# Kernel optimization log

Hardware: AMD Instinct MI355X
Metric: run time of the kernel (lower is better)

Reference implementation:

```python
import jax, jax.numpy as jnp
import numpy as np
import math

N_HEAD = 16  # from init_kwargs

def setup_inputs() -> dict:
    key = jax.random.key(0)
    ks = jax.random.split(key, 11)
    B, T, D = 2, 2048, 1024
    s = 0.02
    return {
        "q": jax.random.normal(ks[0], (B, T, D), jnp.float32),
        "k": jax.random.normal(ks[1], (B, T, D), jnp.float32),
        "v": jax.random.normal(ks[2], (B, T, D), jnp.float32),
        "Wq": jax.random.normal(ks[3], (D, D), jnp.float32) * s,
        "bq": jax.random.normal(ks[4], (D,), jnp.float32) * s,
        "Wk": jax.random.normal(ks[5], (D, D), jnp.float32) * s,
        "bk": jax.random.normal(ks[6], (D,), jnp.float32) * s,
        "Wv": jax.random.normal(ks[7], (D, D), jnp.float32) * s,
        "bv": jax.random.normal(ks[8], (D,), jnp.float32) * s,
        "Wc": jax.random.normal(ks[9], (D, D), jnp.float32) * s,
        "bc": jax.random.normal(ks[10], (D,), jnp.float32) * s,
    }

def reference(q, k, v, Wq, bq, Wk, bk, Wv, bv, Wc, bc):
    B, T, D = q.shape
    H = N_HEAD
    nd = D // H

    def proj(x, W, b):
        # torch Linear: x @ W.T + b; then split heads -> [b, h, t, nd]
        y = x @ W.T + b
        return y.reshape(B, T, H, nd).transpose(0, 2, 1, 3)

    qh = proj(q, Wq, bq)
    kh = proj(k, Wk, bk)
    vh = proj(v, Wv, bv)

    # scores: [b, h, t_q, t_k]
    z = jnp.einsum('bhqd,bhkd->bhqk', qh, kh) / math.sqrt(nd)
    mask = jnp.tril(jnp.ones((T, T), dtype=bool))  # causal
    z = jnp.where(mask, z, -jnp.inf)
    # NOTE: original uses nn.Softmax(dim=-2) -> softmax over the QUERY axis
    attn = jax.nn.softmax(z, axis=-2)
    out = jnp.einsum('bhqk,bhkd->bhqd', attn, vh)  # [b, h, t, nd]
    out = out.transpose(0, 2, 1, 3).reshape(B, T, D)
    return out @ Wc.T + bc
```

## Files before the change

### kernel.cpp

```cpp
#include <hip/hip_runtime.h>


#define Dd 1024
#define Tt 2048
#define Bb 2
#define Hh 16
#define NDh 64
#define Mm (Bb * Tt)

using u16 = unsigned short;
using u32 = unsigned int;
typedef __attribute__((ext_vector_type(8))) short bf16x8;
typedef __attribute__((ext_vector_type(4))) float f32x4;

__device__ __forceinline__ u16 f2bf(float f) {
  return (u16)((__float_as_uint(f) + 0x8000u) >> 16);
}
__device__ __forceinline__ u32 pk2(float a, float b) {
  u32 ua = __float_as_uint(a) + 0x8000u;
  u32 ub = __float_as_uint(b) + 0x8000u;
  return __builtin_amdgcn_perm(ub, ua, 0x07060302u);
}
__device__ __forceinline__ void ldsdma16(const u16* g, u16* l) {
  __builtin_amdgcn_global_load_lds(
      (const __attribute__((address_space(1))) u32*)g,
      (__attribute__((address_space(3))) u32*)l, 16, 0, 0);
}
#define MFMA(a, b, c) __builtin_amdgcn_mfma_f32_16x16x32_bf16((a), (b), (c), 0, 0, 0)
__device__ __forceinline__ bf16x8 ldfrag(const u16* lds, int row, int kgrp) {
  return *(const bf16x8*)(lds + row * 64 + (((kgrp) ^ (row & 7)) * 8));
}

__global__ __launch_bounds__(256) void cvt_w(
    const float* __restrict__ w0, const float* __restrict__ w1,
    const float* __restrict__ w2, const float* __restrict__ w3,
    u16* __restrict__ dst, float* __restrict__ outz, float* __restrict__ lsumz)
{
  const int vid = blockIdx.x * 256 + threadIdx.x;
  const int seg = vid >> 18;
  const int off = (vid & 0x3FFFF) * 4;
  const float* s = seg == 0 ? w0 : seg == 1 ? w1 : seg == 2 ? w2 : w3;
  float4 f = *(const float4*)(s + off);
  ushort4 o;
  o.x = f2bf(f.x); o.y = f2bf(f.y); o.z = f2bf(f.z); o.w = f2bf(f.w);
  *(ushort4*)(dst + (size_t)seg * Dd * Dd + off) = o;
  *(float4*)(outz + (size_t)vid * 4) = make_float4(0.f, 0.f, 0.f, 0.f);
  if (vid < Bb * Hh * Tt / 4)
    *(float4*)(lsumz + (size_t)vid * 4) = make_float4(0.f, 0.f, 0.f, 0.f);
}

template <bool XF32>
__device__ __forceinline__ void gemm_body(
    const void* Xv, const u16* __restrict__ WB, const float* __restrict__ bias,
    void* Yv, float oscale, int omode, int kc, int knum, u16* As, u16* Bs)
{
  const int t = threadIdx.x, lane = t & 63, w = t >> 6;
  const int col = lane & 15, quad = lane >> 4;
  const int m0 = blockIdx.x * 64, n0 = blockIdx.y * 128;
  const int wm = (w >> 1) * 32, wn = (w & 1) * 64;
  const int drr = lane >> 3, dsw = ((lane & 7) ^ drr) * 8;
  const int ar = t >> 2, ag = (t & 3) * 2;
  const int kbeg = (Dd / knum) * kc, kend = kbeg + Dd / knum;

  f32x4 acc[2][4] = {};
  float4 xf[4];
  const float* X32 = (const float*)Xv;
  if constexpr (XF32) {
#pragma unroll
    for (int j = 0; j < 4; j++)
      xf[j] = ((const float4*)(X32 + (size_t)(m0 + ar) * Dd + kbeg + ag * 8))[j];
  }

  for (int k0 = kbeg; k0 < kend; k0 += 64) {
    __syncthreads();
#pragma unroll
    for (int i = 0; i < 4; i++) {
      const int rr = w * 32 + i * 8;
      ldsdma16(WB + (size_t)(n0 + rr + drr) * Dd + k0 + dsw, Bs + rr * 64);
    }
    if constexpr (XF32) {
      u32 pk[8];
#pragma unroll
      for (int j = 0; j < 4; j++) {
        pk[2 * j]     = pk2(xf[j].x, xf[j].y);
        pk[2 * j + 1] = pk2(xf[j].z, xf[j].w);
      }
      u16* dst = As + ar * 64;
      *(uint4*)(dst + ((ag ^ (ar & 7)) * 8))       = make_uint4(pk[0], pk[1], pk[2], pk[3]);
      *(uint4*)(dst + (((ag + 1) ^ (ar & 7)) * 8)) = make_uint4(pk[4], pk[5], pk[6], pk[7]);
      if (k0 + 64 < kend) {
#pragma unroll
        for (int j = 0; j < 4; j++)
          xf[j] = ((const float4*)(X32 + (size_t)(m0 + ar) * Dd + k0 + 64 + ag * 8))[j];
      }
    } else {
      const u16* X = (const u16*)Xv;
#pragma unroll
      for (int i = 0; i < 2; i++) {
        const int rr = w * 16 + i * 8;
        ldsdma16(X + (size_t)(m0 + rr + drr) * Dd + k0 + dsw, As + rr * 64);
      }
    }
    __syncthreads();
#pragma unroll
    for (int s = 0; s < 2; s++) {
      bf16x8 a[2], b[4];
#pragma unroll
      for (int i = 0; i < 2; i++)
        a[i] = ldfrag(As, wm + i * 16 + col, s * 4 + quad);
#pragma unroll
      for (int j = 0; j < 4; j++)
        b[j] = ldfrag(Bs, wn + j * 16 + col, s * 4 + quad);
#pragma unroll
      for (int i = 0; i < 2; i++)
#pragma unroll
        for (int j = 0; j < 4; j++)
          acc[i][j] = MFMA(a[i], b[j], acc[i][j]);
    }
  }

#pragma unroll
  for (int jt = 0; jt < 4; jt++) {
    const int n = n0 + wn + jt * 16 + col;
    const float bn = (omode == 2 && kc != 0) ? 0.f : bias[n];
    if (omode == 1) {
#pragma unroll
      for (int i = 0; i < 2; i++) {
        const int mg = m0 + wm + i * 16 + quad * 4;
        const int bb = mg >> 11, tl = mg & 2047;
        ushort4 o;
        o.x = f2bf(acc[i][jt][0] + bn);
        o.y = f2bf(acc[i][jt][1] + bn);
        o.z = f2bf(acc[i][jt][2] + bn);
        o.w = f2bf(acc[i][jt][3] + bn);
        *(ushort4*)((u16*)Yv + (size_t)bb * Dd * Tt + (size_t)n * Tt + tl) = o;
      }
    } else if (omode == 0) {
      u16* Y = (u16*)Yv;
#pragma unroll
      for (int i = 0; i < 2; i++)
#pragma unroll
        for (int r = 0; r < 4; r++) {
          const int m = m0 + wm + i * 16 + quad * 4 + r;
          Y[(size_t)m * Dd + n] = f2bf((acc[i][jt][r] + bn) * oscale);
        }
    } else {
      float* Y = (float*)Yv;
#pragma unroll
      for (int i = 0; i < 2; i++)
#pragma unroll
        for (int r = 0; r < 4; r++) {
          const int m = m0 + wm + i * 16 + quad * 4 + r;
          atomicAdd(&Y[(size_t)m * Dd + n], acc[i][jt][r] + bn);
        }
    }
  }
}

__global__ __launch_bounds__(256) void proj_qkv(
    const float* __restrict__ q, const float* __restrict__ k,
    const float* __restrict__ v, const u16* __restrict__ Wb,
    const float* __restrict__ bq, const float* __restrict__ bk,
    const float* __restrict__ bv,
    u16* __restrict__ Qp, u16* __restrict__ Kp, u16* __restrict__ VtG)
{
  __shared__ u16 As[64 * 64];
  __shared__ u16 Bs[128 * 64];
  const int z = blockIdx.z;
  const float* X = z == 0 ? q : z == 1 ? k : v;
  const u16* W = Wb + (size_t)z * Dd * Dd;
  const float* bias = z == 0 ? bq : z == 1 ? bk : bv;
  void* Y = z == 0 ? (void*)Qp : z == 1 ? (void*)Kp : (void*)VtG;
  gemm_body<true>(X, W, bias, Y, z == 0 ? 0.125f : 1.0f, z == 2 ? 1 : 0, 0, 1, As, Bs);
}

__global__ __launch_bounds__(256) void gemm_final(
    const u16* __restrict__ Ctx, const u16* __restrict__ Wcb,
    const float* __restrict__ bc, float* __restrict__ out)
{
  __shared__ u16 As[64 * 64];
  __shared__ u16 Bs[128 * 64];
  gemm_body<false>(Ctx, Wcb, bc, out, 1.0f, 2, blockIdx.z, 2, As, Bs);
}

__global__ __launch_bounds__(256) void attn_stats(
    const u16* __restrict__ Qp, const u16* __restrict__ Kp,
    float* __restrict__ lsum)
{
  __shared__ u16 Ks[128 * 64];
  __shared__ u16 Qs[64 * 64];
  const int t = threadIdx.x, lane = t & 63, w = t >> 6;
  const int col = lane & 15, quad = lane >> 4;
  const int bh = blockIdx.x, b = bh >> 4, h = bh & 15;
  const int j = blockIdx.y, tk0 = j * 128, c = blockIdx.z;
  const u16* Kbase = Kp + (size_t)b * Tt * Dd + h * NDh;
  const u16* Qbase = Qp + (size_t)b * Tt * Dd + h * NDh;
  const int drr = lane >> 3, dsw = ((lane & 7) ^ drr) * 8;

#pragma unroll
  for (int i = 0; i < 4; i++) {
    const int rr = w * 32 + i * 8;
    ldsdma16(Kbase + (size_t)(tk0 + rr + drr) * Dd + dsw, Ks + rr * 64);
  }
  __syncthreads();
  bf16x8 ka[2][2];
#pragma unroll
  for (int s2 = 0; s2 < 2; s2++) {
    const int row = w * 32 + s2 * 16 + col;
    ka[s2][0] = ldfrag(Ks, row, quad);
    ka[s2][1] = ldfrag(Ks, row, 4 + quad);
  }

  float l[2][4] = {};

  for (int d = 2 * j + c, i0 = 0; d < Tt / 64; d += 4, i0++) {
    const bool masked = (c < 2) && (i0 == 0);
    const int tq0 = d * 64;
    __syncthreads();
#pragma unroll
    for (int i = 0; i < 2; i++) {
      const int rr = w * 16 + i * 8;
      ldsdma16(Qbase + (size_t)(tq0 + rr + drr) * Dd + dsw, Qs + rr * 64);
    }
    __syncthreads();
#pragma unroll
    for (int jt = 0; jt < 4; jt++) {
      bf16x8 qb0 = ldfrag(Qs, jt * 16 + col, quad);
      bf16x8 qb1 = ldfrag(Qs, jt * 16 + col, 4 + quad);
      const int tq = tq0 + jt * 16 + col;
#pragma unroll
      for (int s2 = 0; s2 < 2; s2++) {
        f32x4 z = {};
        z = MFMA(ka[s2][0], qb0, z);
        z = MFMA(ka[s2][1], qb1, z);
#pragma unroll
        for (int r = 0; r < 4; r++) {
          float e = __expf(z[r]);
          if (masked) {
            const int tk = tk0 + w * 32 + s2 * 16 + quad * 4 + r;
            e = (tq >= tk) ? e : 0.f;
          }
          l[s2][r] += e;
        }
      }
    }
  }

#pragma unroll
  for (int s2 = 0; s2 < 2; s2++)
#pragma unroll
    for (int r = 0; r < 4; r++) {
      float s = l[s2][r];
#pragma unroll
      for (int m = 1; m < 16; m <<= 1) s += __shfl_xor(s, m);
      if (col == 0)
        atomicAdd(&lsum[(size_t)bh * Tt + tk0 + w * 32 + s2 * 16 + quad * 4 + r], s);
    }
}

__global__ __launch_bounds__(256) void attn_out(
    const u16* __restrict__ Qp, const u16* __restrict__ Kp,
    const u16* __restrict__ VtG, const float* __restrict__ lsum,
    u16* __restrict__ Ctx)
{
  __shared__ u16 QPs[64 * 64];
  __shared__ u16 Ks[64 * 64];
  __shared__ u16 Vts[64 * 64];
  __shared__ float srl[64];
  const int t = threadIdx.x, lane = t & 63, w = t >> 6;
  const int col = lane & 15, quad = lane >> 4;
  const int bh = blockIdx.x, b = bh >> 4, h = bh & 15;
  const int tq0 = (gridDim.y - 1 - blockIdx.y) * 64;
  const u16* Qbase = Qp + (size_t)b * Tt * Dd + h * NDh;
  const u16* Kbase = Kp + (size_t)b * Tt * Dd + h * NDh;
  const u16* Vbase = VtG + (size_t)b * Dd * Tt + (size_t)h * NDh * Tt;
  const int drr = lane >> 3, dsw = ((lane & 7) ^ drr) * 8;

#pragma unroll
  for (int i = 0; i < 2; i++) {
    const int rr = w * 16 + i * 8;
    ldsdma16(Qbase + (size_t)(tq0 + rr + drr) * Dd + dsw, QPs + rr * 64);
  }
  __syncthreads();
  bf16x8 qa[2];
  qa[0] = ldfrag(QPs, w * 16 + col, quad);
  qa[1] = ldfrag(QPs, w * 16 + col, 4 + quad);

  f32x4 o[4] = {};

  for (int tk0 = 0; tk0 <= tq0; tk0 += 64) {
    const bool masked = (tk0 == tq0);
    __syncthreads();
#pragma unroll
    for (int i = 0; i < 2; i++) {
      const int rr = w * 16 + i * 8;
      ldsdma16(Kbase + (size_t)(tk0 + rr + drr) * Dd + dsw, Ks + rr * 64);
      ldsdma16(Vbase + (size_t)(rr + drr) * Tt + tk0 + dsw, Vts + rr * 64);
    }
    if (t < 64) srl[t] = 1.0f / lsum[(size_t)bh * Tt + tk0 + t];
    __syncthreads();
#pragma unroll
    for (int jt = 0; jt < 4; jt++) {
      bf16x8 kb0 = ldfrag(Ks, jt * 16 + col, quad);
      bf16x8 kb1 = ldfrag(Ks, jt * 16 + col, 4 + quad);
      const int tkl = jt * 16 + col;
      const float rl = srl[tkl];
      f32x4 z = {};
      z = MFMA(qa[0], kb0, z);
      z = MFMA(qa[1], kb1, z);
#pragma unroll
      for (int r = 0; r < 4; r++) {
        const int row = w * 16 + quad * 4 + r;
        float p = __expf(z[r]) * rl;
        if (masked) p = (tkl <= row) ? p : 0.f;
        QPs[row * 64 + (((tkl >> 3) ^ (row & 7)) * 8) + (tkl & 7)] = f2bf(p);
      }
    }
    bf16x8 pa0 = ldfrag(QPs, w * 16 + col, quad);
    bf16x8 pa1 = ldfrag(QPs, w * 16 + col, 4 + quad);
#pragma unroll
    for (int dn = 0; dn < 4; dn++) {
      bf16x8 vb0 = ldfrag(Vts, dn * 16 + col, quad);
      bf16x8 vb1 = ldfrag(Vts, dn * 16 + col, 4 + quad);
      o[dn] = MFMA(pa0, vb0, o[dn]);
      o[dn] = MFMA(pa1, vb1, o[dn]);
    }
  }

#pragma unroll
  for (int dn = 0; dn < 4; dn++)
#pragma unroll
    for (int r = 0; r < 4; r++) {
      const int tq = tq0 + w * 16 + quad * 4 + r;
      Ctx[(size_t)(b * Tt + tq) * Dd + h * NDh + dn * 16 + col] = f2bf(o[dn][r]);
    }
}

extern "C" void kernel_launch(void* const* d_in, const int* in_sizes, int n_in,
                              void* d_out, int out_size, void* d_ws, size_t ws_size,
                              hipStream_t stream)
{
  const float* q  = (const float*)d_in[0];
  const float* k  = (const float*)d_in[1];
  const float* v  = (const float*)d_in[2];
  const float* Wq = (const float*)d_in[3];
  const float* bq = (const float*)d_in[4];
  const float* Wk = (const float*)d_in[5];
  const float* bk = (const float*)d_in[6];
  const float* Wv = (const float*)d_in[7];
  const float* bv = (const float*)d_in[8];
  const float* Wc = (const float*)d_in[9];
  const float* bc = (const float*)d_in[10];

  u16* Wb   = (u16*)d_ws;
  u16* Qp   = Wb + (size_t)4 * Dd * Dd;
  u16* Kp   = Qp + (size_t)Mm * Dd;
  u16* VtG  = Kp + (size_t)Mm * Dd;
  u16* Ctx  = VtG + (size_t)Mm * Dd;
  float* lsum = (float*)(Ctx + (size_t)Mm * Dd);

  cvt_w<<<4096, 256, 0, stream>>>(Wq, Wk, Wv, Wc, Wb, (float*)d_out, lsum);
  proj_qkv<<<dim3(Mm / 64, Dd / 128, 3), 256, 0, stream>>>(
      q, k, v, Wb, bq, bk, bv, Qp, Kp, VtG);
  attn_stats<<<dim3(Bb * Hh, Tt / 128, 4), 256, 0, stream>>>(Qp, Kp, lsum);
  attn_out<<<dim3(Bb * Hh, Tt / 64), 256, 0, stream>>>(Qp, Kp, VtG, lsum, Ctx);
  gemm_final<<<dim3(Mm / 64, Dd / 128, 2), 256, 0, stream>>>(
      Ctx, Wb + (size_t)3 * Dd * Dd, bc, (float*)d_out);
}
```

Measured before the change: 268.0 us.

## Pre-convert activations to bf16 and use 128x128 GEMM tiles with LDS DMA

Activation conversion from fp32 to bf16 for q/k/v moves into the weight-conversion kernel, so the projection GEMM can load both operands with global-to-LDS DMA instead of register-staged conversion. GEMM tiles for both projection and final GEMMs grow from 64x128 to 128x128, giving each wave a 64x64 sub-tile and more MFMA work per loaded byte. This costs an extra bf16 round trip of the activations through memory and more registers per thread, and it reuses workspace regions (Ctx holds converted v) which must not conflict in time. Grid sizes halve, which lowers the number of concurrent blocks.

```diff
diff --git a/kernel.cpp b/kernel.cpp
--- a/kernel.cpp
+++ b/kernel.cpp
@@ -16,11 +16,6 @@
 __device__ __forceinline__ u16 f2bf(float f) {
   return (u16)((__float_as_uint(f) + 0x8000u) >> 16);
 }
-__device__ __forceinline__ u32 pk2(float a, float b) {
-  u32 ua = __float_as_uint(a) + 0x8000u;
-  u32 ub = __float_as_uint(b) + 0x8000u;
-  return __builtin_amdgcn_perm(ub, ua, 0x07060302u);
-}
 __device__ __forceinline__ void ldsdma16(const u16* g, u16* l) {
   __builtin_amdgcn_global_load_lds(
       (const __attribute__((address_space(1))) u32*)g,
@@ -31,88 +26,72 @@
   return *(const bf16x8*)(lds + row * 64 + (((kgrp) ^ (row & 7)) * 8));
 }
 
-__global__ __launch_bounds__(256) void cvt_w(
+__global__ __launch_bounds__(256) void cvt_all(
     const float* __restrict__ w0, const float* __restrict__ w1,
     const float* __restrict__ w2, const float* __restrict__ w3,
-    u16* __restrict__ dst, float* __restrict__ outz, float* __restrict__ lsumz)
+    const float* __restrict__ xq, const float* __restrict__ xk,
+    const float* __restrict__ xv,
+    u16* __restrict__ Wb, u16* __restrict__ Qb, u16* __restrict__ Kb,
+    u16* __restrict__ Vb, float* __restrict__ outz, float* __restrict__ lsumz)
 {
   const int vid = blockIdx.x * 256 + threadIdx.x;
   const int seg = vid >> 18;
-  const int off = (vid & 0x3FFFF) * 4;
-  const float* s = seg == 0 ? w0 : seg == 1 ? w1 : seg == 2 ? w2 : w3;
+  const size_t off = (size_t)(vid & 0x3FFFF) * 4;
+  const float* s;
+  u16* d;
+  if (seg < 4) {
+    s = seg == 0 ? w0 : seg == 1 ? w1 : seg == 2 ? w2 : w3;
+    d = Wb + (size_t)seg * Dd * Dd;
+  } else {
+    const int xi = (seg - 4) >> 2;
+    const size_t xo = (size_t)((seg - 4) & 3) << 20;
+    s = (xi == 0 ? xq : xi == 1 ? xk : xv) + xo;
+    d = (xi == 0 ? Qb : xi == 1 ? Kb : Vb) + xo;
+  }
   float4 f = *(const float4*)(s + off);
   ushort4 o;
   o.x = f2bf(f.x); o.y = f2bf(f.y); o.z = f2bf(f.z); o.w = f2bf(f.w);
-  *(ushort4*)(dst + (size_t)seg * Dd * Dd + off) = o;
-  *(float4*)(outz + (size_t)vid * 4) = make_float4(0.f, 0.f, 0.f, 0.f);
+  *(ushort4*)(d + off) = o;
+  if (vid < Mm * Dd / 4)
+    *(float4*)(outz + (size_t)vid * 4) = make_float4(0.f, 0.f, 0.f, 0.f);
   if (vid < Bb * Hh * Tt / 4)
     *(float4*)(lsumz + (size_t)vid * 4) = make_float4(0.f, 0.f, 0.f, 0.f);
 }
 
-template <bool XF32>
 __device__ __forceinline__ void gemm_body(
-    const void* Xv, const u16* __restrict__ WB, const float* __restrict__ bias,
-    void* Yv, float oscale, int omode, int kc, int knum, u16* As, u16* Bs)
+    const u16* __restrict__ X, const u16* __restrict__ WB,
+    const float* __restrict__ bias, void* Yv, float oscale, int omode,
+    int kc, int knum, u16* As, u16* Bs)
 {
   const int t = threadIdx.x, lane = t & 63, w = t >> 6;
   const int col = lane & 15, quad = lane >> 4;
-  const int m0 = blockIdx.x * 64, n0 = blockIdx.y * 128;
-  const int wm = (w >> 1) * 32, wn = (w & 1) * 64;
+  const int m0 = blockIdx.x * 128, n0 = blockIdx.y * 128;
+  const int wm = (w >> 1) * 64, wn = (w & 1) * 64;
   const int drr = lane >> 3, dsw = ((lane & 7) ^ drr) * 8;
-  const int ar = t >> 2, ag = (t & 3) * 2;
   const int kbeg = (Dd / knum) * kc, kend = kbeg + Dd / knum;
 
-  f32x4 acc[2][4] = {};
-  float4 xf[4];
-  const float* X32 = (const float*)Xv;
-  if constexpr (XF32) {
-#pragma unroll
-    for (int j = 0; j < 4; j++)
-      xf[j] = ((const float4*)(X32 + (size_t)(m0 + ar) * Dd + kbeg + ag * 8))[j];
-  }
+  f32x4 acc[4][4] = {};
 
   for (int k0 = kbeg; k0 < kend; k0 += 64) {
     __syncthreads();
 #pragma unroll
     for (int i = 0; i < 4; i++) {
       const int rr = w * 32 + i * 8;
+      ldsdma16(X  + (size_t)(m0 + rr + drr) * Dd + k0 + dsw, As + rr * 64);
       ldsdma16(WB + (size_t)(n0 + rr + drr) * Dd + k0 + dsw, Bs + rr * 64);
     }
-    if constexpr (XF32) {
-      u32 pk[8];
-#pragma unroll
-      for (int j = 0; j < 4; j++) {
-        pk[2 * j]     = pk2(xf[j].x, xf[j].y);
-        pk[2 * j + 1] = pk2(xf[j].z, xf[j].w);
-      }
-      u16* dst = As + ar * 64;
-      *(uint4*)(dst + ((ag ^ (ar & 7)) * 8))       = make_uint4(pk[0], pk[1], pk[2], pk[3]);
-      *(uint4*)(dst + (((ag + 1) ^ (ar & 7)) * 8)) = make_uint4(pk[4], pk[5], pk[6], pk[7]);
-      if (k0 + 64 < kend) {
-#pragma unroll
-        for (int j = 0; j < 4; j++)
-          xf[j] = ((const float4*)(X32 + (size_t)(m0 + ar) * Dd + k0 + 64 + ag * 8))[j];
-      }
-    } else {
-      const u16* X = (const u16*)Xv;
-#pragma unroll
-      for (int i = 0; i < 2; i++) {
-        const int rr = w * 16 + i * 8;
-        ldsdma16(X + (size_t)(m0 + rr + drr) * Dd + k0 + dsw, As + rr * 64);
-      }
-    }
     __syncthreads();
 #pragma unroll
     for (int s = 0; s < 2; s++) {
-      bf16x8 a[2], b[4];
-#pragma unroll
-      for (int i = 0; i < 2; i++)
+      bf16x8 a[4], b[4];
+#pragma unroll
+      for (int i = 0; i < 4; i++)
         a[i] = ldfrag(As, wm + i * 16 + col, s * 4 + quad);
 #pragma unroll
       for (int j = 0; j < 4; j++)
         b[j] = ldfrag(Bs, wn + j * 16 + col, s * 4 + quad);
 #pragma unroll
-      for (int i = 0; i < 2; i++)
+      for (int i = 0; i < 4; i++)
 #pragma unroll
         for (int j = 0; j < 4; j++)
           acc[i][j] = MFMA(a[i], b[j], acc[i][j]);
@@ -125,7 +104,7 @@
     const float bn = (omode == 2 && kc != 0) ? 0.f : bias[n];
     if (omode == 1) {
 #pragma unroll
-      for (int i = 0; i < 2; i++) {
+      for (int i = 0; i < 4; i++) {
         const int mg = m0 + wm + i * 16 + quad * 4;
         const int bb = mg >> 11, tl = mg & 2047;
         ushort4 o;
@@ -138,7 +117,7 @@
     } else if (omode == 0) {
       u16* Y = (u16*)Yv;
 #pragma unroll
-      for (int i = 0; i < 2; i++)
+      for (int i = 0; i < 4; i++)
 #pragma unroll
         for (int r = 0; r < 4; r++) {
           const int m = m0 + wm + i * 16 + quad * 4 + r;
@@ -147,7 +126,7 @@
     } else {
       float* Y = (float*)Yv;
 #pragma unroll
-      for (int i = 0; i < 2; i++)
+      for (int i = 0; i < 4; i++)
 #pragma unroll
         for (int r = 0; r < 4; r++) {
           const int m = m0 + wm + i * 16 + quad * 4 + r;
@@ -158,29 +137,29 @@
 }
 
 __global__ __launch_bounds__(256) void proj_qkv(
-    const float* __restrict__ q, const float* __restrict__ k,
-    const float* __restrict__ v, const u16* __restrict__ Wb,
+    const u16* __restrict__ Qb, const u16* __restrict__ Kb,
+    const u16* __restrict__ Vb, const u16* __restrict__ Wb,
     const float* __restrict__ bq, const float* __restrict__ bk,
     const float* __restrict__ bv,
     u16* __restrict__ Qp, u16* __restrict__ Kp, u16* __restrict__ VtG)
 {
-  __shared__ u16 As[64 * 64];
+  __shared__ u16 As[128 * 64];
   __shared__ u16 Bs[128 * 64];
   const int z = blockIdx.z;
-  const float* X = z == 0 ? q : z == 1 ? k : v;
+  const u16* X = z == 0 ? Qb : z == 1 ? Kb : Vb;
   const u16* W = Wb + (size_t)z * Dd * Dd;
   const float* bias = z == 0 ? bq : z == 1 ? bk : bv;
   void* Y = z == 0 ? (void*)Qp : z == 1 ? (void*)Kp : (void*)VtG;
-  gemm_body<true>(X, W, bias, Y, z == 0 ? 0.125f : 1.0f, z == 2 ? 1 : 0, 0, 1, As, Bs);
+  gemm_body(X, W, bias, Y, z == 0 ? 0.125f : 1.0f, z == 2 ? 1 : 0, 0, 1, As, Bs);
 }
 
 __global__ __launch_bounds__(256) void gemm_final(
     const u16* __restrict__ Ctx, const u16* __restrict__ Wcb,
     const float* __restrict__ bc, float* __restrict__ out)
 {
-  __shared__ u16 As[64 * 64];
+  __shared__ u16 As[128 * 64];
   __shared__ u16 Bs[128 * 64];
-  gemm_body<false>(Ctx, Wcb, bc, out, 1.0f, 2, blockIdx.z, 2, As, Bs);
+  gemm_body(Ctx, Wcb, bc, out, 1.0f, 2, blockIdx.z, 2, As, Bs);
 }
 
 __global__ __launch_bounds__(256) void attn_stats(
@@ -358,12 +337,16 @@
   u16* VtG  = Kp + (size_t)Mm * Dd;
   u16* Ctx  = VtG + (size_t)Mm * Dd;
   float* lsum = (float*)(Ctx + (size_t)Mm * Dd);
-
-  cvt_w<<<4096, 256, 0, stream>>>(Wq, Wk, Wv, Wc, Wb, (float*)d_out, lsum);
-  proj_qkv<<<dim3(Mm / 64, Dd / 128, 3), 256, 0, stream>>>(
-      q, k, v, Wb, bq, bk, bv, Qp, Kp, VtG);
+  u16* Qb   = (u16*)(lsum + (size_t)Bb * Hh * Tt);
+  u16* Kb   = Qb + (size_t)Mm * Dd;
+  u16* Vb   = Ctx;
+
+  cvt_all<<<16384, 256, 0, stream>>>(Wq, Wk, Wv, Wc, q, k, v,
+                                     Wb, Qb, Kb, Vb, (float*)d_out, lsum);
+  proj_qkv<<<dim3(Mm / 128, Dd / 128, 3), 256, 0, stream>>>(
+      Qb, Kb, Vb, Wb, bq, bk, bv, Qp, Kp, VtG);
   attn_stats<<<dim3(Bb * Hh, Tt / 128, 4), 256, 0, stream>>>(Qp, Kp, lsum);
   attn_out<<<dim3(Bb * Hh, Tt / 64), 256, 0, stream>>>(Qp, Kp, VtG, lsum, Ctx);
-  gemm_final<<<dim3(Mm / 64, Dd / 128, 2), 256, 0, stream>>>(
+  gemm_final<<<dim3(Mm / 128, Dd / 128, 2), 256, 0, stream>>>(
       Ctx, Wb + (size_t)3 * Dd * Dd, bc, (float*)d_out);
 }
```

Measured after the change: 262.6 us. 1.02x faster.
